# Kernel optimization log

Measured on AMD Instinct MI355X. Metric: run time of the kernel, lower is better.

## Reference

```python
import jax, jax.numpy as jnp
import numpy as np

B, D, H, W = 32, 256, 32, 32
K = 1024
COMMITMENT_COST = 0.25


def setup_inputs() -> dict:
    key = jax.random.key(0)
    k1, k2 = jax.random.split(key)
    z = jax.random.normal(k1, (B, D, H, W), dtype=jnp.float32)
    # torch init: uniform_(-1/K, 1/K)
    emb_weight = jax.random.uniform(k2, (K, D), dtype=jnp.float32,
                                    minval=-1.0 / K, maxval=1.0 / K)
    return {"z": z, "emb_weight": emb_weight}


def reference(z, emb_weight):
    b, c, h, w = z.shape
    # [B, D, H, W] -> [B*H*W, D]
    z_flat = jnp.transpose(z, (0, 2, 3, 1)).reshape(-1, c)
    # squared-distance: ||z||^2 + ||e||^2 - 2 z.e  -> [N, K]
    distances = (jnp.sum(z_flat ** 2, axis=1, keepdims=True)
                 + jnp.sum(emb_weight ** 2, axis=1)[None, :]
                 - 2.0 * jnp.matmul(z_flat, emb_weight.T))
    encoding_indices = jnp.argmin(distances, axis=1)  # [N]
    z_q = emb_weight[encoding_indices]                # [N, D]
    z_q = z_q.reshape(b, h, w, c).transpose(0, 3, 1, 2)  # [B, D, H, W]

    q_latent_loss = jnp.mean((jax.lax.stop_gradient(z_q) - z) ** 2)
    e_latent_loss = jnp.mean((z_q - jax.lax.stop_gradient(z)) ** 2)
    loss = q_latent_loss + COMMITMENT_COST * e_latent_loss

    # straight-through estimator
    z_q = z + jax.lax.stop_gradient(z_q - z)
    return z_q, loss, encoding_indices
```

## Files before the change

kernel.cpp:

```cpp
#include <hip/hip_runtime.h>

#define NPTS  32768
#define DIM   256
#define KCB   1024

#define ZQ_OFF   0
#define LOSS_OFF 8388608
#define IDX_OFF  8388609

typedef __attribute__((ext_vector_type(8))) short short8;
typedef __attribute__((ext_vector_type(4))) float f32x4;

__device__ __forceinline__ int z_base(int n) { return ((n >> 10) << 18) | (n & 1023); }

__device__ __forceinline__ unsigned short f2bf(float f) {
    unsigned u = __float_as_uint(f);
    u += 0x7FFFu + ((u >> 16) & 1u);
    return (unsigned short)(u >> 16);
}

__device__ __forceinline__ unsigned long long pack_vi(float v, int i) {
    unsigned int u = __float_as_uint(v);
    unsigned int key = (u & 0x80000000u) ? ~u : u;
    return ((unsigned long long)key << 32) | (unsigned int)i;
}

__device__ __forceinline__ float np_half_sq(const float* __restrict__ p, int stride) {
    float S[16];
#pragma unroll
    for (int l = 0; l < 16; ++l) {
        float t[8];
#pragma unroll
        for (int j = 0; j < 8; ++j) {
            float v = p[(j * 16 + l) * stride];
            t[j] = __fmul_rn(v, v);
        }
        S[l] = __fadd_rn(__fadd_rn(__fadd_rn(t[0], t[1]), __fadd_rn(t[2], t[3])),
                         __fadd_rn(__fadd_rn(t[4], t[5]), __fadd_rn(t[6], t[7])));
    }
    float u[8];
#pragma unroll
    for (int i = 0; i < 8; ++i) u[i] = __fadd_rn(S[i], S[i + 8]);
    float v4[4];
#pragma unroll
    for (int i = 0; i < 4; ++i) v4[i] = __fadd_rn(u[i], u[i + 4]);
    return __fadd_rn(__fadd_rn(v4[0], v4[2]), __fadd_rn(v4[1], v4[3]));
}
__device__ __forceinline__ float np_sum256_sq(const float* __restrict__ p, int stride) {
    return __fadd_rn(np_half_sq(p, stride), np_half_sq(p + 128 * stride, stride));
}

__global__ __launch_bounds__(256) void setup_kernel(
    const float* __restrict__ z, const float* __restrict__ emb,
    float* __restrict__ z2, float* __restrict__ eps,
    float* __restrict__ e2, float* __restrict__ e2h,
    unsigned short* __restrict__ ebf,
    double* __restrict__ loss_acc, unsigned int* __restrict__ ticket)
{
    if (blockIdx.x < 128) {
        int n = blockIdx.x * 256 + threadIdx.x;
        const float* p = z + z_base(n);
        z2[n] = np_sum256_sq(p, 1024);
        float a = 0.0f;
#pragma unroll 8
        for (int d = 0; d < 256; ++d) a += fabsf(p[d << 10]);
        eps[n] = __builtin_fmaf(1e-5f, a, 3e-4f);
        if (blockIdx.x == 0 && threadIdx.x == 0) { *loss_acc = 0.0; *ticket = 0u; }
    } else {
        int kb = (blockIdx.x - 128) * 256;
        for (int idx = threadIdx.x; idx < 256 * 256; idx += 256) {
            int k = kb + (idx >> 8), d = idx & 255;
            ebf[k * 256 + d] = f2bf(emb[k * 256 + d]);
        }
        int k = kb + threadIdx.x;
        float s = np_sum256_sq(emb + k * DIM, 1);
        e2[k] = s;
        e2h[k] = 0.5f * s;
    }
}

#define ZS_STRIDE 264
#define ES_STRIDE 40
#define ES_SIZE   (128 * ES_STRIDE)

__global__ __launch_bounds__(256) void dist_kernel(
    const float* __restrict__ z, const float* __restrict__ emb,
    const unsigned short* __restrict__ ebf,
    const float* __restrict__ z2w, const float* __restrict__ e2w,
    const float* __restrict__ e2hw, const float* __restrict__ epsw,
    float* __restrict__ out_idx)
{
    __shared__ __align__(16) short zs[64 * ZS_STRIDE];
    __shared__ __align__(16) short es[2 * ES_SIZE];
    __shared__ float redbuf[64 * 32];
    __shared__ int   cl[64 * 32];
    __shared__ float MxS[64], thrS[64], epsS[64], z2S[64];
    __shared__ unsigned int cntS[64];
    __shared__ unsigned long long bestS[64];
    __shared__ int ovfS;

    const int tid = threadIdx.x;
    const int w  = tid >> 6;
    const int l  = tid & 63;
    const int lq = l >> 4;
    const int lr = l & 15;
    const int n0 = blockIdx.x << 6;
    const int zb = z_base(n0);

    if (tid < 64) {
        MxS[tid] = -3.4e38f; thrS[tid] = 3.4e38f;
        cntS[tid] = 0u; bestS[tid] = 0x7FFFFFFFFFFFFFFFULL;
        epsS[tid] = epsw[n0 + tid]; z2S[tid] = z2w[n0 + tid];
    }
    if (tid == 0) ovfS = 0;
    for (int i = tid; i < 64 * 32; i += 256) cl[i] = 0;

    {
        int q = tid & 15, d0 = tid >> 4;
#pragma unroll 4
        for (int i = 0; i < 16; ++i) {
            int d = d0 + 16 * i;
            float4 v = *(const float4*)(z + zb + (d << 10) + 4 * q);
            zs[(4 * q + 0) * ZS_STRIDE + d] = (short)f2bf(v.x);
            zs[(4 * q + 1) * ZS_STRIDE + d] = (short)f2bf(v.y);
            zs[(4 * q + 2) * ZS_STRIDE + d] = (short)f2bf(v.z);
            zs[(4 * q + 3) * ZS_STRIDE + d] = (short)f2bf(v.w);
        }
    }

    const int skk = tid >> 1, sh = tid & 1;

    {
        const int4* src = (const int4*)(ebf + skk * 256 + sh * 16);
        int4 a = src[0], b = src[1];
        int4* dst = (int4*)(es + skk * ES_STRIDE + sh * 16);
        dst[0] = a; dst[1] = b;
    }
    __syncthreads();

    f32x4 acc[2][4];
#pragma unroll
    for (int mt = 0; mt < 2; ++mt)
#pragma unroll
        for (int nt = 0; nt < 4; ++nt) acc[mt][nt] = (f32x4)0.0f;

    const int mrow = 32 * (w & 1);
    const int kwv  = 64 * (w >> 1);

    int4 pa, pb;
#pragma unroll 1
    for (int g = 0; g < 72; ++g) {
        const int kt = g >> 3, dt = g & 7;
        const int k0 = (kt < 8 ? kt : 0) * 128;
        if (g < 71) {
            int gn = g + 1;
            int k0n = ((gn >> 3) < 8 ? (gn >> 3) : 0) * 128;
            const int4* src = (const int4*)(ebf + (k0n + skk) * 256 + (gn & 7) * 32 + sh * 16);
            pa = src[0]; pb = src[1];
        }
        {
            const short* esb = es + (g & 1) * ES_SIZE;
            const int dbase = dt * 32;
            short8 af0 = *(const short8*)(zs + (mrow + lr) * ZS_STRIDE + dbase + lq * 8);
            short8 af1 = *(const short8*)(zs + (mrow + 16 + lr) * ZS_STRIDE + dbase + lq * 8);
#pragma unroll
            for (int nt = 0; nt < 4; ++nt) {
                short8 bf = *(const short8*)(esb + (kwv + 16 * nt + lr) * ES_STRIDE + lq * 8);
                acc[0][nt] = __builtin_amdgcn_mfma_f32_16x16x32_bf16(af0, bf, acc[0][nt], 0, 0, 0);
                acc[1][nt] = __builtin_amdgcn_mfma_f32_16x16x32_bf16(af1, bf, acc[1][nt], 0, 0, 0);
            }
        }
        if (g < 71) {
            int4* dst = (int4*)(es + ((g + 1) & 1) * ES_SIZE + skk * ES_STRIDE + sh * 16);
            dst[0] = pa; dst[1] = pb;
            __syncthreads();
        }
        if (dt == 7) {
            if (g == 71) __syncthreads();
            float e2hr[4]; int kg[4];
#pragma unroll
            for (int nt = 0; nt < 4; ++nt) {
                kg[nt] = k0 + kwv + 16 * nt + lr;
                e2hr[nt] = e2hw[kg[nt]];
            }
            float vals[2][4][4];
#pragma unroll
            for (int mt = 0; mt < 2; ++mt)
#pragma unroll
                for (int nt = 0; nt < 4; ++nt)
#pragma unroll
                    for (int r = 0; r < 4; ++r)
                        vals[mt][nt][r] = acc[mt][nt][r] - e2hr[nt];
            if (kt < 8) {
#pragma unroll
                for (int mt = 0; mt < 2; ++mt)
#pragma unroll
                    for (int r = 0; r < 4; ++r) {
                        float m = fmaxf(fmaxf(vals[mt][0][r], vals[mt][1][r]),
                                        fmaxf(vals[mt][2][r], vals[mt][3][r]));
                        int row = mrow + 16 * mt + lq * 4 + r;
                        redbuf[row * 32 + (w >> 1) * 16 + lr] = m;
                    }
                __syncthreads();
                if (tid < 64) {
                    float m = redbuf[tid * 32];
#pragma unroll 8
                    for (int c = 1; c < 32; ++c) m = fmaxf(m, redbuf[tid * 32 + c]);
                    float Mx = fmaxf(MxS[tid], m);
                    MxS[tid] = Mx;
                    thrS[tid] = Mx - epsS[tid];
                }
                __syncthreads();
            }
            if (kt >= 1) {
#pragma unroll
                for (int mt = 0; mt < 2; ++mt)
#pragma unroll
                    for (int r = 0; r < 4; ++r) {
                        int row = mrow + 16 * mt + lq * 4 + r;
                        float th = thrS[row];
#pragma unroll
                        for (int nt = 0; nt < 4; ++nt) {
                            if (vals[mt][nt][r] >= th) {
                                unsigned int p = atomicAdd(&cntS[row], 1u);
                                if (p < 32u) cl[row * 32 + p] = kg[nt];
                                else atomicMax(&ovfS, 1);
                            }
                        }
                    }
            }
            if (kt < 8) {
#pragma unroll
                for (int mt = 0; mt < 2; ++mt)
#pragma unroll
                    for (int nt = 0; nt < 4; ++nt) acc[mt][nt] = (f32x4)0.0f;
            }
        }
    }

    __syncthreads();
    float* zx = (float*)es;
    const int pt = tid & 63;
    const int s0 = tid >> 6;
    unsigned int nc = cntS[pt]; if (nc > 32u) nc = 32u;
    bool  act[8]; int kE[8]; float accE[8];
#pragma unroll
    for (int j = 0; j < 8; ++j) {
        unsigned int s = (unsigned int)s0 + 4u * j;
        act[j] = s < nc;
        kE[j] = act[j] ? cl[pt * 32 + s] : 0;
        accE[j] = 0.0f;
    }
#pragma unroll 1
    for (int dt = 0; dt < 8; ++dt) {
        const int dbase = dt * 32;
        __syncthreads();
        {
            int q = tid & 15, dd0 = tid >> 4;
            float4 v0 = *(const float4*)(z + zb + ((dbase + dd0) << 10) + 4 * q);
            float4 v1 = *(const float4*)(z + zb + ((dbase + dd0 + 16) << 10) + 4 * q);
            *(float4*)(zx + dd0 * 68 + 4 * q) = v0;
            *(float4*)(zx + (dd0 + 16) * 68 + 4 * q) = v1;
        }
        __syncthreads();
#pragma unroll
        for (int j = 0; j < 8; ++j) {
            if (!act[j]) continue;
            const float* er = emb + kE[j] * 256 + dbase;
            float ev[32];
#pragma unroll
            for (int c = 0; c < 8; ++c) *(float4*)(ev + 4 * c) = *(const float4*)(er + 4 * c);
            float a = accE[j];
#pragma unroll
            for (int dd = 0; dd < 32; ++dd)
                a = __builtin_fmaf(zx[dd * 68 + pt], ev[dd], a);
            accE[j] = a;
        }
    }
#pragma unroll
    for (int j = 0; j < 8; ++j) {
        if (!act[j]) continue;
        int k = kE[j];
        float t1 = __fadd_rn(z2S[pt], e2w[k]);
        float d  = __fsub_rn(t1, __fmul_rn(2.0f, accE[j]));
        atomicMin(&bestS[pt], pack_vi(d, k));
    }
    __syncthreads();

    if (ovfS) {
        for (int row = 0; row < 64; ++row) {
            if (cntS[row] <= 32u) continue;
            float fa[4] = {0.f, 0.f, 0.f, 0.f};
            for (int dt = 0; dt < 8; ++dt) {
                const int dbase = dt * 32;
                __syncthreads();
                {
                    int q = tid & 15, dd0 = tid >> 4;
                    float4 v0 = *(const float4*)(z + zb + ((dbase + dd0) << 10) + 4 * q);
                    float4 v1 = *(const float4*)(z + zb + ((dbase + dd0 + 16) << 10) + 4 * q);
                    *(float4*)(zx + dd0 * 68 + 4 * q) = v0;
                    *(float4*)(zx + (dd0 + 16) * 68 + 4 * q) = v1;
                }
                __syncthreads();
                for (int c = 0; c < 4; ++c) {
                    const float* er = emb + (tid + 256 * c) * 256 + dbase;
                    for (int dd = 0; dd < 32; ++dd)
                        fa[c] = __builtin_fmaf(zx[dd * 68 + row], er[dd], fa[c]);
                }
            }
            for (int c = 0; c < 4; ++c) {
                int k = tid + 256 * c;
                float t1 = __fadd_rn(z2S[row], e2w[k]);
                float d  = __fsub_rn(t1, __fmul_rn(2.0f, fa[c]));
                atomicMin(&bestS[row], pack_vi(d, k));
            }
            __syncthreads();
        }
    }

    if (tid < 64)
        out_idx[n0 + tid] = (float)(unsigned int)(bestS[tid] & 0xFFFFFFFFULL);
}

__global__ __launch_bounds__(256) void zq_loss_kernel(
    const float* __restrict__ z, const float* __restrict__ emb,
    const float* __restrict__ idxv, float* __restrict__ zq,
    double* __restrict__ loss_acc, unsigned int* __restrict__ ticket,
    float* __restrict__ out_loss)
{
    const int n = blockIdx.x * 256 + threadIdx.x;
    const int kk = (int)idxv[n];
    const float* er = emb + kk * DIM;
    const int zb = z_base(n);
    double s = 0.0;
#pragma unroll 8
    for (int d = 0; d < DIM; ++d) {
        float ev = er[d];
        float zv = z[zb + (d << 10)];
        zq[zb + (d << 10)] = ev;
        float df = ev - zv;
        s = fma((double)df, (double)df, s);
    }
    for (int off = 32; off; off >>= 1) s += __shfl_down(s, off, 64);
    __shared__ double sred[4];
    if ((threadIdx.x & 63) == 0) sred[threadIdx.x >> 6] = s;
    __syncthreads();
    if (threadIdx.x == 0) {
        atomicAdd(loss_acc, (sred[0] + sred[1]) + (sred[2] + sred[3]));
        __threadfence();
        unsigned int old = atomicAdd(ticket, 1u);
        if (old == gridDim.x - 1) {
            double total = atomicAdd(loss_acc, 0.0);
            out_loss[0] = (float)(1.25 * (total / 8388608.0));
        }
    }
}

extern "C" void kernel_launch(void* const* d_in, const int* in_sizes, int n_in,
                              void* d_out, int out_size, void* d_ws, size_t ws_size,
                              hipStream_t stream) {
    const float* z   = (const float*)d_in[0];
    const float* emb = (const float*)d_in[1];
    float* out = (float*)d_out;

    float* z2w = (float*)d_ws;
    float* epsw = (float*)((char*)d_ws + 131072);
    float* e2w = (float*)((char*)d_ws + 262144);
    float* e2hw = (float*)((char*)d_ws + 266240);
    unsigned short* ebf = (unsigned short*)((char*)d_ws + 270336);
    double* loss_acc = (double*)((char*)d_ws + 794624);
    unsigned int* ticket = (unsigned int*)((char*)d_ws + 794632);

    setup_kernel<<<132, 256, 0, stream>>>(z, emb, z2w, epsw, e2w, e2hw, ebf,
                                          loss_acc, ticket);
    dist_kernel<<<NPTS / 64, 256, 0, stream>>>(z, emb, ebf, z2w, e2w, e2hw, epsw,
                                               out + IDX_OFF);
    zq_loss_kernel<<<NPTS / 256, 256, 0, stream>>>(z, emb, out + IDX_OFF,
                                                   out + ZQ_OFF, loss_acc, ticket,
                                                   out + LOSS_OFF);
}
```

Measured before the change: 248.1 us.

## Restructure codebook distance GEMM with async LDS loads, register-held z tiles, swizzled layout

The codebook bf16 copy is pre-swizzled into per-wave tile chunks so each wave streams its own 64-code slice through a triple-buffered LDS ring using global_load_lds with vmcnt waits, replacing block-wide double buffering and per-step __syncthreads. The z tile fragments for all 256 dims are held in registers, and accumulators start at -||e||^2/2 so the per-tile subtraction disappears. The running-max threshold is computed only once from the first code tile, with shuffle reductions, and candidates are gathered afterwards. Setup fuses the abs-sum into the squared-norm pass, and the zq/loss kernel splits each point across two threads to get more blocks. The cost is much higher register pressure and a looser threshold taken from a single tile, which may push more candidates into the exact rescoring path.

```diff
diff --git a/kernel.cpp b/kernel.cpp
--- a/kernel.cpp
+++ b/kernel.cpp
@@ -10,19 +10,21 @@
 
 typedef __attribute__((ext_vector_type(8))) short short8;
 typedef __attribute__((ext_vector_type(4))) float f32x4;
+typedef unsigned short ushort_t;
+typedef unsigned int u32;
 
 __device__ __forceinline__ int z_base(int n) { return ((n >> 10) << 18) | (n & 1023); }
 
-__device__ __forceinline__ unsigned short f2bf(float f) {
-    unsigned u = __float_as_uint(f);
+__device__ __forceinline__ ushort_t f2bf(float f) {
+    u32 u = __float_as_uint(f);
     u += 0x7FFFu + ((u >> 16) & 1u);
-    return (unsigned short)(u >> 16);
+    return (ushort_t)(u >> 16);
 }
 
 __device__ __forceinline__ unsigned long long pack_vi(float v, int i) {
-    unsigned int u = __float_as_uint(v);
-    unsigned int key = (u & 0x80000000u) ? ~u : u;
-    return ((unsigned long long)key << 32) | (unsigned int)i;
+    u32 u = __float_as_uint(v);
+    u32 key = (u & 0x80000000u) ? ~u : u;
+    return ((unsigned long long)key << 32) | (u32)i;
 }
 
 __device__ __forceinline__ float np_half_sq(const float* __restrict__ p, int stride) {
@@ -48,29 +50,62 @@
 }
 __device__ __forceinline__ float np_sum256_sq(const float* __restrict__ p, int stride) {
     return __fadd_rn(np_half_sq(p, stride), np_half_sq(p + 128 * stride, stride));
+}
+
+__device__ __forceinline__ float np_half_sq_abs(const float* __restrict__ p, int stride, float* aacc) {
+    float S[16]; float a = *aacc;
+#pragma unroll
+    for (int l = 0; l < 16; ++l) {
+        float t[8];
+#pragma unroll
+        for (int j = 0; j < 8; ++j) {
+            float v = p[(j * 16 + l) * stride];
+            t[j] = __fmul_rn(v, v);
+            a = __fadd_rn(a, fabsf(v));
+        }
+        S[l] = __fadd_rn(__fadd_rn(__fadd_rn(t[0], t[1]), __fadd_rn(t[2], t[3])),
+                         __fadd_rn(__fadd_rn(t[4], t[5]), __fadd_rn(t[6], t[7])));
+    }
+    float u[8];
+#pragma unroll
+    for (int i = 0; i < 8; ++i) u[i] = __fadd_rn(S[i], S[i + 8]);
+    float v4[4];
+#pragma unroll
+    for (int i = 0; i < 4; ++i) v4[i] = __fadd_rn(u[i], u[i + 4]);
+    *aacc = a;
+    return __fadd_rn(__fadd_rn(v4[0], v4[2]), __fadd_rn(v4[1], v4[3]));
 }
 
 __global__ __launch_bounds__(256) void setup_kernel(
     const float* __restrict__ z, const float* __restrict__ emb,
     float* __restrict__ z2, float* __restrict__ eps,
     float* __restrict__ e2, float* __restrict__ e2h,
-    unsigned short* __restrict__ ebf,
+    ushort_t* __restrict__ ebf,
     double* __restrict__ loss_acc, unsigned int* __restrict__ ticket)
 {
     if (blockIdx.x < 128) {
         int n = blockIdx.x * 256 + threadIdx.x;
         const float* p = z + z_base(n);
-        z2[n] = np_sum256_sq(p, 1024);
         float a = 0.0f;
-#pragma unroll 8
-        for (int d = 0; d < 256; ++d) a += fabsf(p[d << 10]);
+        float h0 = np_half_sq_abs(p, 1024, &a);
+        float h1 = np_half_sq_abs(p + 128 * 1024, 1024, &a);
+        z2[n] = __fadd_rn(h0, h1);
         eps[n] = __builtin_fmaf(1e-5f, a, 3e-4f);
         if (blockIdx.x == 0 && threadIdx.x == 0) { *loss_acc = 0.0; *ticket = 0u; }
     } else {
         int kb = (blockIdx.x - 128) * 256;
-        for (int idx = threadIdx.x; idx < 256 * 256; idx += 256) {
-            int k = kb + (idx >> 8), d = idx & 255;
-            ebf[k * 256 + d] = f2bf(emb[k * 256 + d]);
+        for (int i = threadIdx.x; i < 8192; i += 256) {
+            int c = i >> 8, s = i & 255;
+            int kcl = c >> 3, dtc = c & 7;
+            int row = s >> 2, sl = s & 3;
+            int lq = sl ^ ((row >> 1) & 3);
+            int k = kb + (kcl << 6) + row;
+            int d0 = dtc * 32 + lq * 8;
+            const float* e = emb + k * 256 + d0;
+            short8 ov;
+#pragma unroll
+            for (int j = 0; j < 8; ++j) ov[j] = (short)f2bf(e[j]);
+            *(short8*)(ebf + ((((kb >> 6) + kcl) << 3) + dtc) * 2048 + (s << 3)) = ov;
         }
         int k = kb + threadIdx.x;
         float s = np_sum256_sq(emb + k * DIM, 1);
@@ -80,23 +115,33 @@
 }
 
 #define ZS_STRIDE 264
-#define ES_STRIDE 40
-#define ES_SIZE   (128 * ES_STRIDE)
-
-__global__ __launch_bounds__(256) void dist_kernel(
+
+__device__ __forceinline__ void async_cp16(const ushort_t* g, ushort_t* l) {
+    __builtin_amdgcn_global_load_lds(
+        (const __attribute__((address_space(1))) u32*)g,
+        (__attribute__((address_space(3))) u32*)l, 16, 0, 0);
+}
+
+#define WAITVM8 asm volatile("s_waitcnt vmcnt(8)" ::: "memory")
+#define WAITVM4 asm volatile("s_waitcnt vmcnt(4)" ::: "memory")
+#define WAITVM0 asm volatile("s_waitcnt vmcnt(0)" ::: "memory")
+#define WAITLG0 asm volatile("s_waitcnt lgkmcnt(0)" ::: "memory")
+#define MEMBAR  asm volatile("" ::: "memory")
+
+__global__ __launch_bounds__(256, 2) void dist_kernel(
     const float* __restrict__ z, const float* __restrict__ emb,
-    const unsigned short* __restrict__ ebf,
+    const ushort_t* __restrict__ ebf,
     const float* __restrict__ z2w, const float* __restrict__ e2w,
     const float* __restrict__ e2hw, const float* __restrict__ epsw,
     float* __restrict__ out_idx)
 {
-    __shared__ __align__(16) short zs[64 * ZS_STRIDE];
-    __shared__ __align__(16) short es[2 * ES_SIZE];
-    __shared__ float redbuf[64 * 32];
-    __shared__ int   cl[64 * 32];
-    __shared__ float MxS[64], thrS[64], epsS[64], z2S[64];
+    __shared__ __align__(16) short uni[24576];
+    __shared__ float e2hS[1024];
+    __shared__ float maxred[256];
+    __shared__ float thrS[64], epsS[64], z2S[64];
     __shared__ unsigned int cntS[64];
     __shared__ unsigned long long bestS[64];
+    __shared__ int cl[64 * 32];
     __shared__ int ovfS;
 
     const int tid = threadIdx.x;
@@ -104,18 +149,22 @@
     const int l  = tid & 63;
     const int lq = l >> 4;
     const int lr = l & 15;
+    const int sw8 = ((lq ^ ((lr >> 1) & 3)) << 3);
     const int n0 = blockIdx.x << 6;
     const int zb = z_base(n0);
+    const int wq = w << 8;
+    const int wbase = w * 6144;
 
     if (tid < 64) {
-        MxS[tid] = -3.4e38f; thrS[tid] = 3.4e38f;
         cntS[tid] = 0u; bestS[tid] = 0x7FFFFFFFFFFFFFFFULL;
         epsS[tid] = epsw[n0 + tid]; z2S[tid] = z2w[n0 + tid];
     }
     if (tid == 0) ovfS = 0;
     for (int i = tid; i < 64 * 32; i += 256) cl[i] = 0;
+    for (int i = tid; i < 1024; i += 256) e2hS[i] = e2hw[i];
 
     {
+        short* zs = uni;
         int q = tid & 15, d0 = tid >> 4;
 #pragma unroll 4
         for (int i = 0; i < 16; ++i) {
@@ -127,119 +176,160 @@
             zs[(4 * q + 3) * ZS_STRIDE + d] = (short)f2bf(v.w);
         }
     }
-
-    const int skk = tid >> 1, sh = tid & 1;
-
+    __syncthreads();
+
+    short8 af[4][8];
     {
-        const int4* src = (const int4*)(ebf + skk * 256 + sh * 16);
-        int4 a = src[0], b = src[1];
-        int4* dst = (int4*)(es + skk * ES_STRIDE + sh * 16);
-        dst[0] = a; dst[1] = b;
+        const short* zs = uni;
+#pragma unroll
+        for (int mt = 0; mt < 4; ++mt)
+#pragma unroll
+            for (int d8 = 0; d8 < 8; ++d8)
+                af[mt][d8] = *(const short8*)(zs + (16 * mt + lr) * ZS_STRIDE + d8 * 32 + lq * 8);
+    }
+
+    f32x4 acc[4][4];
+#pragma unroll
+    for (int nt = 0; nt < 4; ++nt) {
+        float e = e2hS[wq + 16 * nt + lr];
+        f32x4 iv = { -e, -e, -e, -e };
+#pragma unroll
+        for (int mt = 0; mt < 4; ++mt) acc[mt][nt] = iv;
     }
     __syncthreads();
 
-    f32x4 acc[2][4];
-#pragma unroll
-    for (int mt = 0; mt < 2; ++mt)
-#pragma unroll
-        for (int nt = 0; nt < 4; ++nt) acc[mt][nt] = (f32x4)0.0f;
-
-    const int mrow = 32 * (w & 1);
-    const int kwv  = 64 * (w >> 1);
-
-    int4 pa, pb;
+    {
+        const int kc0 = (w << 2);
+#pragma unroll
+        for (int c = 0; c < 3; ++c) {
+            const ushort_t* gs = ebf + (((kc0 << 3) + c) * 2048) + (l << 3);
+            ushort_t* ld = (ushort_t*)(uni + wbase + c * 2048);
+            async_cp16(gs,        ld);
+            async_cp16(gs +  512, ld +  512);
+            async_cp16(gs + 1024, ld + 1024);
+            async_cp16(gs + 1536, ld + 1536);
+        }
+    }
+    WAITVM8;
+    short8 c0, c1, c2, c3;
+    {
+        const short* esb = uni + wbase;
+        c0 = *(const short8*)(esb + ( 0 + lr) * 32 + sw8);
+        c1 = *(const short8*)(esb + (16 + lr) * 32 + sw8);
+        c2 = *(const short8*)(esb + (32 + lr) * 32 + sw8);
+        c3 = *(const short8*)(esb + (48 + lr) * 32 + sw8);
+    }
+
+    int bufr = 0;
 #pragma unroll 1
-    for (int g = 0; g < 72; ++g) {
-        const int kt = g >> 3, dt = g & 7;
-        const int k0 = (kt < 8 ? kt : 0) * 128;
-        if (g < 71) {
-            int gn = g + 1;
-            int k0n = ((gn >> 3) < 8 ? (gn >> 3) : 0) * 128;
-            const int4* src = (const int4*)(ebf + (k0n + skk) * 256 + (gn & 7) * 32 + sh * 16);
-            pa = src[0]; pb = src[1];
-        }
-        {
-            const short* esb = es + (g & 1) * ES_SIZE;
-            const int dbase = dt * 32;
-            short8 af0 = *(const short8*)(zs + (mrow + lr) * ZS_STRIDE + dbase + lq * 8);
-            short8 af1 = *(const short8*)(zs + (mrow + 16 + lr) * ZS_STRIDE + dbase + lq * 8);
-#pragma unroll
-            for (int nt = 0; nt < 4; ++nt) {
-                short8 bf = *(const short8*)(esb + (kwv + 16 * nt + lr) * ES_STRIDE + lq * 8);
-                acc[0][nt] = __builtin_amdgcn_mfma_f32_16x16x32_bf16(af0, bf, acc[0][nt], 0, 0, 0);
-                acc[1][nt] = __builtin_amdgcn_mfma_f32_16x16x32_bf16(af1, bf, acc[1][nt], 0, 0, 0);
-            }
-        }
-        if (g < 71) {
-            int4* dst = (int4*)(es + ((g + 1) & 1) * ES_SIZE + skk * ES_STRIDE + sh * 16);
-            dst[0] = pa; dst[1] = pb;
-            __syncthreads();
-        }
-        if (dt == 7) {
-            if (g == 71) __syncthreads();
-            float e2hr[4]; int kg[4];
-#pragma unroll
-            for (int nt = 0; nt < 4; ++nt) {
-                kg[nt] = k0 + kwv + 16 * nt + lr;
-                e2hr[nt] = e2hw[kg[nt]];
-            }
-            float vals[2][4][4];
-#pragma unroll
-            for (int mt = 0; mt < 2; ++mt)
-#pragma unroll
-                for (int nt = 0; nt < 4; ++nt)
+    for (int kt = 0; kt < 5; ++kt) {
+        const bool kt4 = (kt == 4);
+        const int ktr = kt4 ? 0 : kt;
+        const int kb = wq + (ktr << 6);
+#pragma unroll
+        for (int dt = 0; dt < 8; ++dt) {
+            const int bufr1 = (bufr == 2) ? 0 : bufr + 1;
+            WAITLG0;
+            if (!kt4 || dt < 5) {
+                const int dtn = (dt + 3) & 7;
+                const int ktn = (dt >= 5) ? kt + 1 : kt;
+                const int kcn = (w << 2) + ((ktn < 4) ? ktn : 0);
+                const ushort_t* gs = ebf + (((kcn << 3) + dtn) * 2048) + (l << 3);
+                ushort_t* ld = (ushort_t*)(uni + wbase + bufr * 2048);
+                async_cp16(gs,        ld);
+                async_cp16(gs +  512, ld +  512);
+                async_cp16(gs + 1024, ld + 1024);
+                async_cp16(gs + 1536, ld + 1536);
+            }
+            if (!kt4 || dt < 5) { WAITVM8; }
+            else if (dt == 5)   { WAITVM4; }
+            else                { WAITVM0; }
+            short8 n0r, n1r, n2r, n3r;
+            if (!kt4 || dt < 7) {
+                const short* esb = uni + wbase + bufr1 * 2048;
+                n0r = *(const short8*)(esb + ( 0 + lr) * 32 + sw8);
+                n1r = *(const short8*)(esb + (16 + lr) * 32 + sw8);
+                n2r = *(const short8*)(esb + (32 + lr) * 32 + sw8);
+                n3r = *(const short8*)(esb + (48 + lr) * 32 + sw8);
+            }
+            __builtin_amdgcn_s_setprio(1);
+#pragma unroll
+            for (int mt = 0; mt < 4; ++mt) {
+                acc[mt][0] = __builtin_amdgcn_mfma_f32_16x16x32_bf16(af[mt][dt], c0, acc[mt][0], 0, 0, 0);
+                acc[mt][1] = __builtin_amdgcn_mfma_f32_16x16x32_bf16(af[mt][dt], c1, acc[mt][1], 0, 0, 0);
+                acc[mt][2] = __builtin_amdgcn_mfma_f32_16x16x32_bf16(af[mt][dt], c2, acc[mt][2], 0, 0, 0);
+                acc[mt][3] = __builtin_amdgcn_mfma_f32_16x16x32_bf16(af[mt][dt], c3, acc[mt][3], 0, 0, 0);
+            }
+            __builtin_amdgcn_s_setprio(0);
+            if (!kt4 || dt < 7) { c0 = n0r; c1 = n1r; c2 = n2r; c3 = n3r; }
+            bufr = bufr1;
+        }
+
+        if (kt == 0) {
+            float mx[4][4];
+#pragma unroll
+            for (int mt = 0; mt < 4; ++mt)
+#pragma unroll
+                for (int r = 0; r < 4; ++r)
+                    mx[mt][r] = fmaxf(fmaxf(acc[mt][0][r], acc[mt][1][r]),
+                                      fmaxf(acc[mt][2][r], acc[mt][3][r]));
+#pragma unroll
+            for (int s = 1; s <= 8; s <<= 1)
+#pragma unroll
+                for (int mt = 0; mt < 4; ++mt)
 #pragma unroll
                     for (int r = 0; r < 4; ++r)
-                        vals[mt][nt][r] = acc[mt][nt][r] - e2hr[nt];
-            if (kt < 8) {
-#pragma unroll
-                for (int mt = 0; mt < 2; ++mt)
-#pragma unroll
-                    for (int r = 0; r < 4; ++r) {
-                        float m = fmaxf(fmaxf(vals[mt][0][r], vals[mt][1][r]),
-                                        fmaxf(vals[mt][2][r], vals[mt][3][r]));
-                        int row = mrow + 16 * mt + lq * 4 + r;
-                        redbuf[row * 32 + (w >> 1) * 16 + lr] = m;
-                    }
-                __syncthreads();
-                if (tid < 64) {
-                    float m = redbuf[tid * 32];
-#pragma unroll 8
-                    for (int c = 1; c < 32; ++c) m = fmaxf(m, redbuf[tid * 32 + c]);
-                    float Mx = fmaxf(MxS[tid], m);
-                    MxS[tid] = Mx;
-                    thrS[tid] = Mx - epsS[tid];
-                }
-                __syncthreads();
-            }
-            if (kt >= 1) {
-#pragma unroll
-                for (int mt = 0; mt < 2; ++mt)
-#pragma unroll
-                    for (int r = 0; r < 4; ++r) {
-                        int row = mrow + 16 * mt + lq * 4 + r;
-                        float th = thrS[row];
-#pragma unroll
-                        for (int nt = 0; nt < 4; ++nt) {
-                            if (vals[mt][nt][r] >= th) {
+                        mx[mt][r] = fmaxf(mx[mt][r], __shfl_xor(mx[mt][r], s, 64));
+#pragma unroll
+            for (int mt = 0; mt < 4; ++mt)
+#pragma unroll
+                for (int r = 0; r < 4; ++r)
+                    if (lr == mt * 4 + r)
+                        maxred[(16 * mt + 4 * lq + r) * 4 + w] = mx[mt][r];
+            WAITLG0; __builtin_amdgcn_s_barrier(); MEMBAR;
+            if (tid < 64) {
+                float a = fmaxf(fmaxf(maxred[tid * 4 + 0], maxred[tid * 4 + 1]),
+                                fmaxf(maxred[tid * 4 + 2], maxred[tid * 4 + 3]));
+                thrS[tid] = a - epsS[tid];
+            }
+            WAITLG0; __builtin_amdgcn_s_barrier(); MEMBAR;
+        } else {
+#pragma unroll
+            for (int mt = 0; mt < 4; ++mt)
+#pragma unroll
+                for (int r = 0; r < 4; ++r) {
+                    int row = 16 * mt + 4 * lq + r;
+                    float th = thrS[row];
+                    float m4 = fmaxf(fmaxf(acc[mt][0][r], acc[mt][1][r]),
+                                     fmaxf(acc[mt][2][r], acc[mt][3][r]));
+                    if (m4 >= th) {
+#pragma unroll
+                        for (int nt = 0; nt < 4; ++nt)
+                            if (acc[mt][nt][r] >= th) {
+                                int kk = kb + 16 * nt + lr;
                                 unsigned int p = atomicAdd(&cntS[row], 1u);
-                                if (p < 32u) cl[row * 32 + p] = kg[nt];
+                                if (p < 32u) cl[row * 32 + p] = kk;
                                 else atomicMax(&ovfS, 1);
                             }
-                        }
                     }
-            }
-            if (kt < 8) {
-#pragma unroll
-                for (int mt = 0; mt < 2; ++mt)
-#pragma unroll
-                    for (int nt = 0; nt < 4; ++nt) acc[mt][nt] = (f32x4)0.0f;
+                }
+        }
+
+        if (kt < 4) {
+            const int nb = kt + 1;
+            const int kbn = wq + ((nb < 4 ? nb : 0) << 6);
+#pragma unroll
+            for (int nt = 0; nt < 4; ++nt) {
+                float e = e2hS[kbn + 16 * nt + lr];
+                f32x4 iv = { -e, -e, -e, -e };
+#pragma unroll
+                for (int mt = 0; mt < 4; ++mt) acc[mt][nt] = iv;
             }
         }
     }
 
     __syncthreads();
-    float* zx = (float*)es;
+    float* zx = (float*)uni;
     const int pt = tid & 63;
     const int s0 = tid >> 6;
     unsigned int nc = cntS[pt]; if (nc > 32u) nc = 32u;
@@ -328,16 +418,18 @@
     double* __restrict__ loss_acc, unsigned int* __restrict__ ticket,
     float* __restrict__ out_loss)
 {
-    const int n = blockIdx.x * 256 + threadIdx.x;
+    const int tl = threadIdx.x & 127;
+    const int h  = threadIdx.x >> 7;
+    const int n  = blockIdx.x * 128 + tl;
     const int kk = (int)idxv[n];
-    const float* er = emb + kk * DIM;
-    const int zb = z_base(n);
+    const float* er = emb + kk * DIM + (h << 7);
+    const int zb2 = z_base(n) + (h << 17);
     double s = 0.0;
 #pragma unroll 8
-    for (int d = 0; d < DIM; ++d) {
-        float ev = er[d];
-        float zv = z[zb + (d << 10)];
-        zq[zb + (d << 10)] = ev;
+    for (int dd = 0; dd < 128; ++dd) {
+        float ev = er[dd];
+        float zv = z[zb2 + (dd << 10)];
+        zq[zb2 + (dd << 10)] = ev;
         float df = ev - zv;
         s = fma((double)df, (double)df, s);
     }
@@ -367,7 +459,7 @@
     float* epsw = (float*)((char*)d_ws + 131072);
     float* e2w = (float*)((char*)d_ws + 262144);
     float* e2hw = (float*)((char*)d_ws + 266240);
-    unsigned short* ebf = (unsigned short*)((char*)d_ws + 270336);
+    ushort_t* ebf = (ushort_t*)((char*)d_ws + 270336);
     double* loss_acc = (double*)((char*)d_ws + 794624);
     unsigned int* ticket = (unsigned int*)((char*)d_ws + 794632);
 
@@ -375,7 +467,7 @@
                                           loss_acc, ticket);
     dist_kernel<<<NPTS / 64, 256, 0, stream>>>(z, emb, ebf, z2w, e2w, e2hw, epsw,
                                                out + IDX_OFF);
-    zq_loss_kernel<<<NPTS / 256, 256, 0, stream>>>(z, emb, out + IDX_OFF,
-                                                   out + ZQ_OFF, loss_acc, ticket,
-                                                   out + LOSS_OFF);
-}
+    zq_loss_kernel<<<256, 256, 0, stream>>>(z, emb, out + IDX_OFF,
+                                            out + ZQ_OFF, loss_acc, ticket,
+                                            out + LOSS_OFF);
+}
```

Measured after the change: 417.6 us. 1.68x slower.
